# Kernel optimization log

Hardware: AMD Instinct MI355X
Metric: run time of the kernel (lower is better)

Reference implementation:

```python
import jax, jax.numpy as jnp
import numpy as np

B, T, C = 4, 2048, 2048
H = 16
D = C // H  # head_dim = 128


def setup_inputs() -> dict:
    key = jax.random.key(0)
    ks = jax.random.split(key, 11)
    s = 0.02
    return {
        "q": jax.random.normal(ks[0], (B, T, C), jnp.float32),
        "k": jax.random.normal(ks[1], (B, T, C), jnp.float32),
        "v": jax.random.normal(ks[2], (B, T, C), jnp.float32),
        "Wq": jax.random.normal(ks[3], (C, C), jnp.float32) * s,
        "bq": jnp.zeros((C,), jnp.float32),
        "Wk": jax.random.normal(ks[4], (C, C), jnp.float32) * s,
        "bk": jnp.zeros((C,), jnp.float32),
        "Wv": jax.random.normal(ks[5], (C, C), jnp.float32) * s,
        "bv": jnp.zeros((C,), jnp.float32),
        "Wo": jax.random.normal(ks[6], (C, C), jnp.float32) * s,
        "bo": jnp.zeros((C,), jnp.float32),
    }


def reference(q, k, v, Wq, bq, Wk, bk, Wv, bv, Wo, bo):
    # torch Linear: y = x @ W.T + b
    def heads(x, W, b):
        y = x @ W.T + b                      # [B,T,C]
        return y.reshape(B, T, H, D).transpose(0, 2, 1, 3)  # [B,H,T,D]

    q_h = heads(q, Wq, bq)
    k_h = heads(k, Wk, bk)
    v_h = heads(v, Wv, bv)

    scale = D ** -0.5
    scores = jnp.einsum('bhqd,bhkd->bhqk', q_h, k_h) * scale  # [B,H,T,T]
    # causal mask (is_causal=True)
    causal = jnp.tril(jnp.ones((T, T), dtype=bool))
    scores = jnp.where(causal, scores, -jnp.inf)
    probs = jax.nn.softmax(scores, axis=-1)
    out = jnp.einsum('bhqk,bhkd->bhqd', probs, v_h)           # [B,H,T,D]
    out = out.transpose(0, 2, 1, 3).reshape(B, T, C)
    return out @ Wo.T + bo
```

## Files before the change

### kernel.cpp

```cpp
#include <hip/hip_runtime.h>
#include <hip/hip_bf16.h>
#include <cmath>


#define DEV __device__ __forceinline__

typedef short short8 __attribute__((ext_vector_type(8)));
typedef float floatx4 __attribute__((ext_vector_type(4)));

#define LDS16(gp, lp)                                                        \
  __builtin_amdgcn_global_load_lds(                                          \
      (const __attribute__((address_space(1))) void*)(gp),                   \
      (__attribute__((address_space(3))) void*)(lp), 16, 0, 0)

DEV unsigned short f2bf(float f) {
  unsigned u = __builtin_bit_cast(unsigned, f);
  u += 0x7fffu + ((u >> 16) & 1u);
  return (unsigned short)(u >> 16);
}

DEV floatx4 mfma16(short8 a, short8 b, floatx4 c) {
  return __builtin_amdgcn_mfma_f32_16x16x32_bf16(a, b, c, 0, 0, 0);
}

struct Cvt7Args {
  const float* in[7];
  unsigned short* out[7];
  int n4[7];
};

__global__ __launch_bounds__(256) void cvt7_kernel(Cvt7Args a) {
  const int s = blockIdx.y;
  const float* __restrict__ in = a.in[s];
  unsigned short* __restrict__ out = a.out[s];
  const int n4 = a.n4[s];
  int stride = gridDim.x * blockDim.x;
  for (int i = blockIdx.x * blockDim.x + threadIdx.x; i < n4; i += stride) {
    float4 v = reinterpret_cast<const float4*>(in)[i];
    ushort4 o;
    o.x = f2bf(v.x); o.y = f2bf(v.y); o.z = f2bf(v.z); o.w = f2bf(v.w);
    reinterpret_cast<ushort4*>(out)[i] = o;
  }
}

DEV void gemm256_core(const unsigned short* __restrict__ aT,
                      const unsigned short* __restrict__ bT,
                      unsigned short* lds, const int K, floatx4 (&acc)[8][4]) {
  const int t = threadIdx.x;
  const int l = t & 63;
  const int w = t >> 6;
  const int wm = w >> 2, wn = w & 3;
  const int lr = l & 15, lg = l >> 4;
  const int NT = K >> 5;

  const int rA0 = t >> 2;
  const int chA0 = (t & 3) ^ ((rA0 >> 1) & 3);
  const int rA1 = (t + 512) >> 2;
  const int chA1 = (t & 3) ^ ((rA1 >> 1) & 3);

  auto stage = [&](int kt, int buf) {
    unsigned short* dst = lds + buf * 16384;
    const unsigned short* ga = aT + kt * 32;
    const unsigned short* gb = bT + kt * 32;
    LDS16(ga + (size_t)rA0 * K + chA0 * 8, dst + t * 8);
    LDS16(ga + (size_t)rA1 * K + chA1 * 8, dst + (t + 512) * 8);
    LDS16(gb + (size_t)rA0 * K + chA0 * 8, dst + 8192 + t * 8);
    LDS16(gb + (size_t)rA1 * K + chA1 * 8, dst + 8192 + (t + 512) * 8);
  };

  stage(0, 0);
  stage(1, 1);
  stage(2, 2);
  asm volatile("s_waitcnt vmcnt(8)" ::: "memory");
  __builtin_amdgcn_s_barrier();
  asm volatile("" ::: "memory");

  for (int tt = 0; tt < NT; ++tt) {
    const unsigned short* lA = lds + (tt & 3) * 16384;
    const unsigned short* lB = lA + 8192;
    if (tt + 3 < NT) stage(tt + 3, (tt + 3) & 3);
    short8 aF[8], bF[4];
#pragma unroll
    for (int ni = 0; ni < 4; ni++) {
      int row = wn * 64 + ni * 16 + lr;
      bF[ni] = *(const short8*)&lB[row * 32 + ((lg ^ ((row >> 1) & 3)) * 8)];
    }
#pragma unroll
    for (int mi = 0; mi < 8; mi++) {
      int row = wm * 128 + mi * 16 + lr;
      aF[mi] = *(const short8*)&lA[row * 32 + ((lg ^ ((row >> 1) & 3)) * 8)];
    }
    __builtin_amdgcn_s_setprio(1);
#pragma unroll
    for (int mi = 0; mi < 8; mi++)
#pragma unroll
      for (int ni = 0; ni < 4; ni++)
        acc[mi][ni] = mfma16(aF[mi], bF[ni], acc[mi][ni]);
    __builtin_amdgcn_s_setprio(0);
    if (tt + 1 < NT) {
      if (tt + 4 <= NT)
        asm volatile("s_waitcnt vmcnt(8)" ::: "memory");
      else if (tt + 3 == NT)
        asm volatile("s_waitcnt vmcnt(4)" ::: "memory");
      else
        asm volatile("s_waitcnt vmcnt(0)" ::: "memory");
      __builtin_amdgcn_s_barrier();
      asm volatile("" ::: "memory");
    }
  }
}

__global__ __launch_bounds__(512, 2) void gemm256_proj3(
    const unsigned short* __restrict__ qb, const unsigned short* __restrict__ kb,
    const unsigned short* __restrict__ vb, const unsigned short* __restrict__ wqb,
    const unsigned short* __restrict__ wkb, const unsigned short* __restrict__ wvb,
    const float* __restrict__ bq, const float* __restrict__ bk,
    const float* __restrict__ bv, unsigned short* __restrict__ Qp,
    unsigned short* __restrict__ Kp, unsigned short* __restrict__ Vt,
    float qscale) {
  constexpr int K = 2048, N = 2048;
  __shared__ unsigned short lds[65536];
  const int seg = blockIdx.x >> 8;
  int inner = blockIdx.x & 255;
  inner = (inner & 7) * 32 + (inner >> 3);
  const int bm = inner >> 3, bn = inner & 7;

  const unsigned short* A = (seg == 0) ? qb : (seg == 1) ? kb : vb;
  const unsigned short* Bw = (seg == 0) ? wqb : (seg == 1) ? wkb : wvb;
  const float* bias = (seg == 0) ? bq : (seg == 1) ? bk : bv;

  floatx4 zero = {0.f, 0.f, 0.f, 0.f};
  floatx4 acc[8][4];
#pragma unroll
  for (int i = 0; i < 8; i++)
#pragma unroll
    for (int j = 0; j < 4; j++) acc[i][j] = zero;

  gemm256_core(A + (size_t)bm * 256 * K, Bw + (size_t)bn * 256 * K, lds, K, acc);

  const int t = threadIdx.x, l = t & 63, w = t >> 6;
  const int wm = w >> 2, wn = w & 3;
  const int lr = l & 15, lg = l >> 4;
  const float oscale = (seg == 0) ? qscale : 1.0f;
  char* ldsb = (char*)lds;

  __syncthreads();

  if (seg < 2) {
#pragma unroll
    for (int ni = 0; ni < 4; ni++) {
      int col = wn * 64 + ni * 16 + lr;
      float bvv = bias[bn * 256 + col];
#pragma unroll
      for (int mi = 0; mi < 8; mi++) {
        int row0 = wm * 128 + mi * 16 + lg * 4;
#pragma unroll
        for (int r = 0; r < 4; r++) {
          int row = row0 + r;
          int off = row * 512 + ((col * 2) ^ (((row >> 2) & 15) << 5));
          *(unsigned short*)(ldsb + off) =
              f2bf((acc[mi][ni][r] + bvv) * oscale);
        }
      }
    }
    __syncthreads();
    unsigned short* dst = (seg == 0) ? Qp : Kp;
#pragma unroll
    for (int i = 0; i < 16; i++) {
      int c = i * 512 + t;
      int row = c >> 5, j = c & 31;
      int off = row * 512 + ((j * 16) ^ (((row >> 2) & 15) << 5));
      short8 v = *(const short8*)(ldsb + off);
      *(short8*)&dst[(size_t)(bm * 256 + row) * N + bn * 256 + j * 8] = v;
    }
  } else {
#pragma unroll
    for (int ni = 0; ni < 4; ni++) {
      int dp = wn * 64 + ni * 16 + lr;
      float bvv = bias[bn * 256 + dp];
#pragma unroll
      for (int mi = 0; mi < 8; mi++) {
        int tp0 = wm * 128 + mi * 16 + lg * 4;
        ushort4 v4;
        v4.x = f2bf(acc[mi][ni][0] + bvv);
        v4.y = f2bf(acc[mi][ni][1] + bvv);
        v4.z = f2bf(acc[mi][ni][2] + bvv);
        v4.w = f2bf(acc[mi][ni][3] + bvv);
        int off = dp * 512 + ((tp0 * 2) ^ ((dp & 15) << 5));
        *(ushort4*)(ldsb + off) = v4;
      }
    }
    __syncthreads();
    const int bb = bm >> 3;
    const int tb = (bm & 7) * 256;
#pragma unroll
    for (int i = 0; i < 16; i++) {
      int c = i * 512 + t;
      int dp = c >> 5, j = c & 31;
      int off = dp * 512 + ((j * 16) ^ ((dp & 15) << 5));
      short8 v = *(const short8*)(ldsb + off);
      int gcd = bn * 256 + dp;
      int h = gcd >> 7, d = gcd & 127;
      *(short8*)&Vt[((size_t)(bb * 16 + h) << 18) + (d << 11) + tb + j * 8] = v;
    }
  }
}

__global__ __launch_bounds__(512, 2) void gemm256_out(
    const unsigned short* __restrict__ A, const unsigned short* __restrict__ Bw,
    const float* __restrict__ bias, float* __restrict__ outp) {
  constexpr int K = 2048, N = 2048;
  __shared__ unsigned short lds[65536];
  int inner = blockIdx.x;
  inner = (inner & 7) * 32 + (inner >> 3);
  const int bm = inner >> 3, bn = inner & 7;

  floatx4 zero = {0.f, 0.f, 0.f, 0.f};
  floatx4 acc[8][4];
#pragma unroll
  for (int i = 0; i < 8; i++)
#pragma unroll
    for (int j = 0; j < 4; j++) acc[i][j] = zero;

  gemm256_core(A + (size_t)bm * 256 * K, Bw + (size_t)bn * 256 * K, lds, K, acc);

  const int t = threadIdx.x, l = t & 63, w = t >> 6;
  const int wm = w >> 2, wn = w & 3;
  const int lr = l & 15, lg = l >> 4;
  char* ldsb = (char*)lds;

  __syncthreads();

#pragma unroll
  for (int half = 0; half < 2; ++half) {
    if (wm == half) {
#pragma unroll
      for (int ni = 0; ni < 4; ni++) {
        int col = wn * 64 + ni * 16 + lr;
        float bvv = bias[bn * 256 + col];
#pragma unroll
        for (int mi = 0; mi < 8; mi++) {
          int lrow0 = mi * 16 + lg * 4;
#pragma unroll
          for (int r = 0; r < 4; r++) {
            int row = lrow0 + r;
            int off = row * 1024 + ((col * 4) ^ (((row >> 2) & 7) << 5));
            *(float*)(ldsb + off) = acc[mi][ni][r] + bvv;
          }
        }
      }
    }
    __syncthreads();
#pragma unroll
    for (int i = 0; i < 16; i++) {
      int c = i * 512 + t;
      int row = c >> 6, j = c & 63;
      int off = row * 1024 + ((j * 16) ^ (((row >> 2) & 7) << 5));
      float4 v = *(const float4*)(ldsb + off);
      *(float4*)&outp[(size_t)(bm * 256 + half * 128 + row) * N + bn * 256 +
                      j * 4] = v;
    }
    __syncthreads();
  }
}

__global__ __launch_bounds__(512, 2) void attn_kernel(
    const unsigned short* __restrict__ Qp, const unsigned short* __restrict__ Kp,
    const unsigned short* __restrict__ Vt, unsigned short* __restrict__ Out) {
  constexpr int T = 2048, C = 2048;
  __shared__ unsigned short lds[49152];
  unsigned short* sP = lds + 32768;

  const int bid = blockIdx.x;
  const int swz = (bid & 7) * 32 + (bid >> 3);
  const int bh = swz >> 2;
  const int pr = swz & 3;
  const int b = bh >> 4, h = bh & 15;
  const int t = threadIdx.x, l = t & 63, w = t >> 6;
  const int lr = l & 15, lg = l >> 4, l7 = l & 7;

  const unsigned short* Kg = Kp + (size_t)(b * T) * C + h * 128;
  const unsigned short* Vg = Vt + ((size_t)bh << 18);

  auto stage_kv = [&](int kb, int buf) {
    unsigned short* dK = lds + (buf ? 8192 : 0);
    unsigned short* dV = lds + 16384 + (buf ? 8192 : 0);
#pragma unroll
    for (int i = 0; i < 2; i++) {
      int c = t + i * 512;
      int row = c >> 4, cc = c & 15;
      LDS16(Kg + (size_t)(kb + row) * C + (cc ^ (row & 7)) * 8, &dK[c * 8]);
    }
#pragma unroll
    for (int i = 0; i < 2; i++) {
      int c = t + i * 512;
      int d = c >> 3, cc = c & 7;
      LDS16(Vg + (size_t)d * T + kb + (cc ^ (d & 7)) * 8, &dV[c * 8]);
    }
  };

  for (int seg = 0; seg < 2; seg++) {
    const int qs = seg ? pr : 7 - pr;
    const unsigned short* Qg = Qp + (size_t)(b * T + qs * 256) * C + h * 128;

#pragma unroll
    for (int i = 0; i < 8; i++) {
      int c = t + i * 512;
      int row = c >> 4, cc = c & 15;
      LDS16(Qg + (size_t)row * C + cc * 8, &lds[c * 8]);
    }
    __syncthreads();
    const int qw = qs * 256 + w * 32;
    short8 qf[2][4];
#pragma unroll
    for (int mi = 0; mi < 2; mi++)
#pragma unroll
      for (int ks = 0; ks < 4; ks++)
        qf[mi][ks] = *(const short8*)&lds[(w * 32 + mi * 16 + lr) * 128 +
                                          ks * 32 + lg * 8];
    __syncthreads();

    floatx4 zero = {0.f, 0.f, 0.f, 0.f};
    floatx4 oacc[2][8];
#pragma unroll
    for (int i = 0; i < 2; i++)
#pragma unroll
      for (int j = 0; j < 8; j++) oacc[i][j] = zero;
    float mold[2][4], lsum[2][4];
#pragma unroll
    for (int i = 0; i < 2; i++)
#pragma unroll
      for (int r = 0; r < 4; r++) { mold[i][r] = -1e30f; lsum[i][r] = 0.f; }

    const int ntile = 4 * qs + 4;
    stage_kv(0, 0);
    __syncthreads();
    int cur = 0;
    for (int tile = 0; tile < ntile; tile++) {
      const int kbase = tile * 64;
      if (tile + 1 < ntile) stage_kv(kbase + 64, cur ^ 1);
      const unsigned short* sK = lds + (cur ? 8192 : 0);
      const unsigned short* sV = lds + 16384 + (cur ? 8192 : 0);
      if (kbase <= qw + 31) {
        floatx4 sc[2][4];
#pragma unroll
        for (int i = 0; i < 2; i++)
#pragma unroll
          for (int j = 0; j < 4; j++) sc[i][j] = zero;
        __builtin_amdgcn_s_setprio(1);
#pragma unroll
        for (int ks = 0; ks < 4; ks++) {
#pragma unroll
          for (int ni = 0; ni < 4; ni++) {
            int R = ni * 16 + lr;
            short8 bF = *(const short8*)&sK[R * 128 + ((ks * 4 + lg) ^ l7) * 8];
#pragma unroll
            for (int mi = 0; mi < 2; mi++)
              sc[mi][ni] = mfma16(qf[mi][ks], bF, sc[mi][ni]);
          }
        }
        __builtin_amdgcn_s_setprio(0);
        if (kbase + 63 > qw) {
#pragma unroll
          for (int mi = 0; mi < 2; mi++)
#pragma unroll
            for (int ni = 0; ni < 4; ni++)
#pragma unroll
              for (int r = 0; r < 4; r++) {
                int col = kbase + ni * 16 + lr;
                int row = qw + mi * 16 + lg * 4 + r;
                if (col > row) sc[mi][ni][r] = -1e30f;
              }
        }
#pragma unroll
        for (int mi = 0; mi < 2; mi++) {
          float xr[4];
          int dok = 1;
#pragma unroll
          for (int r = 0; r < 4; r++) {
            float x = fmaxf(fmaxf(sc[mi][0][r], sc[mi][1][r]),
                            fmaxf(sc[mi][2][r], sc[mi][3][r]));
            x = fmaxf(x, __shfl_xor(x, 1));
            x = fmaxf(x, __shfl_xor(x, 2));
            x = fmaxf(x, __shfl_xor(x, 4));
            x = fmaxf(x, __shfl_xor(x, 8));
            xr[r] = x;
            dok &= (x - mold[mi][r] <= 8.0f) ? 1 : 0;
          }
          const bool defer = __all(dok);
          float al[4];
          if (!defer) {
#pragma unroll
            for (int r = 0; r < 4; r++) {
              float m2 = fmaxf(mold[mi][r], xr[r]);
              al[r] = __builtin_amdgcn_exp2f(mold[mi][r] - m2);
              mold[mi][r] = m2;
            }
          }
          float rs[4] = {0.f, 0.f, 0.f, 0.f};
#pragma unroll
          for (int ni = 0; ni < 4; ni++)
#pragma unroll
            for (int r = 0; r < 4; r++) {
              float p = __builtin_amdgcn_exp2f(sc[mi][ni][r] - mold[mi][r]);
              sc[mi][ni][r] = p;
              rs[r] += p;
            }
#pragma unroll
          for (int r = 0; r < 4; r++) {
            float s = rs[r];
            s += __shfl_xor(s, 1);
            s += __shfl_xor(s, 2);
            s += __shfl_xor(s, 4);
            s += __shfl_xor(s, 8);
            rs[r] = s;
          }
          if (!defer) {
#pragma unroll
            for (int r = 0; r < 4; r++)
              lsum[mi][r] = lsum[mi][r] * al[r] + rs[r];
#pragma unroll
            for (int ni = 0; ni < 8; ni++)
#pragma unroll
              for (int r = 0; r < 4; r++) oacc[mi][ni][r] *= al[r];
          } else {
#pragma unroll
            for (int r = 0; r < 4; r++) lsum[mi][r] += rs[r];
          }
#pragma unroll
          for (int ni = 0; ni < 4; ni++)
#pragma unroll
            for (int r = 0; r < 4; r++) {
              int rr = mi * 16 + lg * 4 + r;
              int ch = (ni * 2 + ((l >> 3) & 1)) ^ (rr & 7);
              sP[w * 2048 + rr * 64 + ch * 8 + l7] = f2bf(sc[mi][ni][r]);
            }
        }
        __builtin_amdgcn_s_setprio(1);
#pragma unroll
        for (int ks = 0; ks < 2; ks++) {
          short8 pf[2];
#pragma unroll
          for (int mi = 0; mi < 2; mi++)
            pf[mi] = *(const short8*)&sP[w * 2048 + (mi * 16 + lr) * 64 +
                                         ((ks * 4 + lg) ^ l7) * 8];
#pragma unroll
          for (int ni = 0; ni < 8; ni++) {
            int d = ni * 16 + lr;
            short8 vF = *(const short8*)&sV[d * 64 + ((ks * 4 + lg) ^ l7) * 8];
#pragma unroll
            for (int mi = 0; mi < 2; mi++)
              oacc[mi][ni] = mfma16(pf[mi], vF, oacc[mi][ni]);
          }
        }
        __builtin_amdgcn_s_setprio(0);
      }
      __syncthreads();
      cur ^= 1;
    }
    {
      char* ldsb = (char*)lds;
#pragma unroll
      for (int mi = 0; mi < 2; mi++) {
        float rl[4];
#pragma unroll
        for (int r = 0; r < 4; r++) rl[r] = 1.0f / lsum[mi][r];
#pragma unroll
        for (int ni = 0; ni < 8; ni++) {
          int col = ni * 16 + lr;
#pragma unroll
          for (int r = 0; r < 4; r++) {
            int row = w * 32 + mi * 16 + lg * 4 + r;
            int off = row * 256 + ((col * 2) ^ (((row >> 2) & 7) << 5));
            *(unsigned short*)(ldsb + off) = f2bf(oacc[mi][ni][r] * rl[r]);
          }
        }
      }
      __syncthreads();
      unsigned short* Og = Out + (size_t)(b * T + qs * 256) * C + h * 128;
#pragma unroll
      for (int i = 0; i < 8; i++) {
        int c = i * 512 + t;
        int row = c >> 4, j = c & 15;
        int off = row * 256 + ((j * 16) ^ (((row >> 2) & 7) << 5));
        short8 v = *(const short8*)(ldsb + off);
        *(short8*)&Og[(size_t)row * C + j * 8] = v;
      }
      __syncthreads();
    }
  }
}

extern "C" void kernel_launch(void* const* d_in, const int* in_sizes, int n_in,
                              void* d_out, int out_size, void* d_ws,
                              size_t ws_size, hipStream_t stream) {
  const float* q = (const float*)d_in[0];
  const float* k = (const float*)d_in[1];
  const float* v = (const float*)d_in[2];
  const float* Wq = (const float*)d_in[3];
  const float* bq = (const float*)d_in[4];
  const float* Wk = (const float*)d_in[5];
  const float* bk = (const float*)d_in[6];
  const float* Wv = (const float*)d_in[7];
  const float* bv = (const float*)d_in[8];
  const float* Wo = (const float*)d_in[9];
  const float* bo = (const float*)d_in[10];

  const int B = 4, T = 2048, C = 2048;
  const size_t E = (size_t)B * T * C;
  const size_t WE = (size_t)C * C;
  unsigned short* ws = (unsigned short*)d_ws;
  unsigned short* qb = ws;
  unsigned short* kb = ws + E;
  unsigned short* vb = ws + 2 * E;
  unsigned short* wqb = ws + 3 * E;
  unsigned short* wkb = wqb + WE;
  unsigned short* wvb = wqb + 2 * WE;
  unsigned short* wob = wqb + 3 * WE;
  unsigned short* Qp = ws + 4 * E;
  unsigned short* Kp = ws + 5 * E;
  unsigned short* Vtb = ws + 6 * E;
  unsigned short* attn = qb;

  Cvt7Args ca;
  ca.in[0] = q;  ca.out[0] = qb;  ca.n4[0] = (int)(E / 4);
  ca.in[1] = k;  ca.out[1] = kb;  ca.n4[1] = (int)(E / 4);
  ca.in[2] = v;  ca.out[2] = vb;  ca.n4[2] = (int)(E / 4);
  ca.in[3] = Wq; ca.out[3] = wqb; ca.n4[3] = (int)(WE / 4);
  ca.in[4] = Wk; ca.out[4] = wkb; ca.n4[4] = (int)(WE / 4);
  ca.in[5] = Wv; ca.out[5] = wvb; ca.n4[5] = (int)(WE / 4);
  ca.in[6] = Wo; ca.out[6] = wob; ca.n4[6] = (int)(WE / 4);
  cvt7_kernel<<<dim3(512, 7), 256, 0, stream>>>(ca);

  const float qscale = 1.4426950408889634f / sqrtf(128.0f);
  gemm256_proj3<<<768, 512, 0, stream>>>(qb, kb, vb, wqb, wkb, wvb, bq, bk, bv,
                                         Qp, Kp, Vtb, qscale);

  attn_kernel<<<256, 512, 0, stream>>>(Qp, Kp, Vtb, attn);

  gemm256_out<<<256, 512, 0, stream>>>(attn, wob, bo, (float*)d_out);
}
```

Before: 492.6 us.

## Split attention into one q-block per workgroup and shrink P staging for occupancy

The attention kernel no longer loops over two causal-balanced q-segments per workgroup. It launches 512 workgroups, each handling a single 256-row q block, with a remapped block index so that long and short segments interleave. The per-wave P staging buffer is halved by writing and consuming P in two 32-column phases, which cuts LDS to 80KB. Launch bounds are raised to 4 waves-per-EU to allow more resident blocks. The costs are more pressure on registers and the loss of the paired load balancing inside each block, which now depends on the hardware scheduler.

```diff
diff --git a/kernel.cpp b/kernel.cpp
--- a/kernel.cpp
+++ b/kernel.cpp
@@ -264,20 +264,23 @@
   }
 }
 
-__global__ __launch_bounds__(512, 2) void attn_kernel(
+__global__ __launch_bounds__(512, 4) void attn_kernel(
     const unsigned short* __restrict__ Qp, const unsigned short* __restrict__ Kp,
     const unsigned short* __restrict__ Vt, unsigned short* __restrict__ Out) {
   constexpr int T = 2048, C = 2048;
-  __shared__ unsigned short lds[49152];
-  unsigned short* sP = lds + 32768;
+  __shared__ unsigned short lds[40960];
 
   const int bid = blockIdx.x;
-  const int swz = (bid & 7) * 32 + (bid >> 3);
-  const int bh = swz >> 2;
-  const int pr = swz & 3;
+  const int u = (bid & 7) * 64 + (bid >> 3);
+  const int p = (u >> 6) * 32 + (u & 31);
+  const int g = (u >> 5) & 1;
+  const int bh = p >> 2;
+  const int pr = p & 3;
+  const int qs = g ? pr : 7 - pr;
   const int b = bh >> 4, h = bh & 15;
   const int t = threadIdx.x, l = t & 63, w = t >> 6;
   const int lr = l & 15, lg = l >> 4, l7 = l & 7;
+  unsigned short* sPw = lds + 32768 + w * 1024;
 
   const unsigned short* Kg = Kp + (size_t)(b * T) * C + h * 128;
   const unsigned short* Vg = Vt + ((size_t)bh << 18);
@@ -299,194 +302,196 @@
     }
   };
 
-  for (int seg = 0; seg < 2; seg++) {
-    const int qs = seg ? pr : 7 - pr;
-    const unsigned short* Qg = Qp + (size_t)(b * T + qs * 256) * C + h * 128;
-
+  const unsigned short* Qg = Qp + (size_t)(b * T + qs * 256) * C + h * 128;
+
+#pragma unroll
+  for (int i = 0; i < 8; i++) {
+    int c = t + i * 512;
+    int row = c >> 4, cc = c & 15;
+    LDS16(Qg + (size_t)row * C + cc * 8, &lds[c * 8]);
+  }
+  __syncthreads();
+  const int qw = qs * 256 + w * 32;
+  short8 qf[2][4];
+#pragma unroll
+  for (int mi = 0; mi < 2; mi++)
+#pragma unroll
+    for (int ks = 0; ks < 4; ks++)
+      qf[mi][ks] = *(const short8*)&lds[(w * 32 + mi * 16 + lr) * 128 +
+                                        ks * 32 + lg * 8];
+  __syncthreads();
+
+  floatx4 zero = {0.f, 0.f, 0.f, 0.f};
+  floatx4 oacc[2][8];
+#pragma unroll
+  for (int i = 0; i < 2; i++)
+#pragma unroll
+    for (int j = 0; j < 8; j++) oacc[i][j] = zero;
+  float mold[2][4], lsum[2][4];
+#pragma unroll
+  for (int i = 0; i < 2; i++)
+#pragma unroll
+    for (int r = 0; r < 4; r++) { mold[i][r] = -1e30f; lsum[i][r] = 0.f; }
+
+  const int ntile = 4 * qs + 4;
+  stage_kv(0, 0);
+  __syncthreads();
+  int cur = 0;
+  for (int tile = 0; tile < ntile; tile++) {
+    const int kbase = tile * 64;
+    if (tile + 1 < ntile) stage_kv(kbase + 64, cur ^ 1);
+    const unsigned short* sK = lds + (cur ? 8192 : 0);
+    const unsigned short* sV = lds + 16384 + (cur ? 8192 : 0);
+    if (kbase <= qw + 31) {
+      floatx4 sc[2][4];
+#pragma unroll
+      for (int i = 0; i < 2; i++)
+#pragma unroll
+        for (int j = 0; j < 4; j++) sc[i][j] = zero;
+      __builtin_amdgcn_s_setprio(1);
+#pragma unroll
+      for (int ks = 0; ks < 4; ks++) {
+#pragma unroll
+        for (int ni = 0; ni < 4; ni++) {
+          int R = ni * 16 + lr;
+          short8 bF = *(const short8*)&sK[R * 128 + ((ks * 4 + lg) ^ l7) * 8];
+#pragma unroll
+          for (int mi = 0; mi < 2; mi++)
+            sc[mi][ni] = mfma16(qf[mi][ks], bF, sc[mi][ni]);
+        }
+      }
+      __builtin_amdgcn_s_setprio(0);
+      if (kbase + 63 > qw) {
+#pragma unroll
+        for (int mi = 0; mi < 2; mi++)
+#pragma unroll
+          for (int ni = 0; ni < 4; ni++)
+#pragma unroll
+            for (int r = 0; r < 4; r++) {
+              int col = kbase + ni * 16 + lr;
+              int row = qw + mi * 16 + lg * 4 + r;
+              if (col > row) sc[mi][ni][r] = -1e30f;
+            }
+      }
+#pragma unroll
+      for (int mi = 0; mi < 2; mi++) {
+        float xr[4];
+        int dok = 1;
+#pragma unroll
+        for (int r = 0; r < 4; r++) {
+          float x = fmaxf(fmaxf(sc[mi][0][r], sc[mi][1][r]),
+                          fmaxf(sc[mi][2][r], sc[mi][3][r]));
+          x = fmaxf(x, __shfl_xor(x, 1));
+          x = fmaxf(x, __shfl_xor(x, 2));
+          x = fmaxf(x, __shfl_xor(x, 4));
+          x = fmaxf(x, __shfl_xor(x, 8));
+          xr[r] = x;
+          dok &= (x - mold[mi][r] <= 8.0f) ? 1 : 0;
+        }
+        const bool defer = __all(dok);
+        float al[4];
+        if (!defer) {
+#pragma unroll
+          for (int r = 0; r < 4; r++) {
+            float m2 = fmaxf(mold[mi][r], xr[r]);
+            al[r] = __builtin_amdgcn_exp2f(mold[mi][r] - m2);
+            mold[mi][r] = m2;
+          }
+        }
+        float rs[4] = {0.f, 0.f, 0.f, 0.f};
+#pragma unroll
+        for (int ni = 0; ni < 4; ni++)
+#pragma unroll
+          for (int r = 0; r < 4; r++) {
+            float p2 = __builtin_amdgcn_exp2f(sc[mi][ni][r] - mold[mi][r]);
+            sc[mi][ni][r] = p2;
+            rs[r] += p2;
+          }
+#pragma unroll
+        for (int r = 0; r < 4; r++) {
+          float s = rs[r];
+          s += __shfl_xor(s, 1);
+          s += __shfl_xor(s, 2);
+          s += __shfl_xor(s, 4);
+          s += __shfl_xor(s, 8);
+          rs[r] = s;
+        }
+        if (!defer) {
+#pragma unroll
+          for (int r = 0; r < 4; r++)
+            lsum[mi][r] = lsum[mi][r] * al[r] + rs[r];
+#pragma unroll
+          for (int ni = 0; ni < 8; ni++)
+#pragma unroll
+            for (int r = 0; r < 4; r++) oacc[mi][ni][r] *= al[r];
+        } else {
+#pragma unroll
+          for (int r = 0; r < 4; r++) lsum[mi][r] += rs[r];
+        }
+      }
+      __builtin_amdgcn_s_setprio(1);
+#pragma unroll
+      for (int ph = 0; ph < 2; ph++) {
+#pragma unroll
+        for (int mi = 0; mi < 2; mi++)
+#pragma unroll
+          for (int dn = 0; dn < 2; dn++)
+#pragma unroll
+            for (int r = 0; r < 4; r++) {
+              int ni = ph * 2 + dn;
+              int rr = mi * 16 + lg * 4 + r;
+              int lch = (dn * 2 + (lr >> 3)) ^ ((rr >> 1) & 3);
+              sPw[rr * 32 + lch * 8 + l7] = f2bf(sc[mi][ni][r]);
+            }
+        short8 pf[2];
+#pragma unroll
+        for (int mi = 0; mi < 2; mi++) {
+          int rr2 = mi * 16 + lr;
+          pf[mi] =
+              *(const short8*)&sPw[rr2 * 32 + ((lg ^ ((rr2 >> 1) & 3)) * 8)];
+        }
+#pragma unroll
+        for (int ni = 0; ni < 8; ni++) {
+          int d = ni * 16 + lr;
+          short8 vF =
+              *(const short8*)&sV[d * 64 + (((ph * 4 + lg) ^ l7) * 8)];
+#pragma unroll
+          for (int mi = 0; mi < 2; mi++)
+            oacc[mi][ni] = mfma16(pf[mi], vF, oacc[mi][ni]);
+        }
+      }
+      __builtin_amdgcn_s_setprio(0);
+    }
+    __syncthreads();
+    cur ^= 1;
+  }
+  {
+    char* ldsb = (char*)lds;
+#pragma unroll
+    for (int mi = 0; mi < 2; mi++) {
+      float rl[4];
+#pragma unroll
+      for (int r = 0; r < 4; r++) rl[r] = 1.0f / lsum[mi][r];
+#pragma unroll
+      for (int ni = 0; ni < 8; ni++) {
+        int col = ni * 16 + lr;
+#pragma unroll
+        for (int r = 0; r < 4; r++) {
+          int row = w * 32 + mi * 16 + lg * 4 + r;
+          int off = row * 256 + ((col * 2) ^ (((row >> 2) & 7) << 5));
+          *(unsigned short*)(ldsb + off) = f2bf(oacc[mi][ni][r] * rl[r]);
+        }
+      }
+    }
+    __syncthreads();
+    unsigned short* Og = Out + (size_t)(b * T + qs * 256) * C + h * 128;
 #pragma unroll
     for (int i = 0; i < 8; i++) {
-      int c = t + i * 512;
-      int row = c >> 4, cc = c & 15;
-      LDS16(Qg + (size_t)row * C + cc * 8, &lds[c * 8]);
-    }
-    __syncthreads();
-    const int qw = qs * 256 + w * 32;
-    short8 qf[2][4];
-#pragma unroll
-    for (int mi = 0; mi < 2; mi++)
-#pragma unroll
-      for (int ks = 0; ks < 4; ks++)
-        qf[mi][ks] = *(const short8*)&lds[(w * 32 + mi * 16 + lr) * 128 +
-                                          ks * 32 + lg * 8];
-    __syncthreads();
-
-    floatx4 zero = {0.f, 0.f, 0.f, 0.f};
-    floatx4 oacc[2][8];
-#pragma unroll
-    for (int i = 0; i < 2; i++)
-#pragma unroll
-      for (int j = 0; j < 8; j++) oacc[i][j] = zero;
-    float mold[2][4], lsum[2][4];
-#pragma unroll
-    for (int i = 0; i < 2; i++)
-#pragma unroll
-      for (int r = 0; r < 4; r++) { mold[i][r] = -1e30f; lsum[i][r] = 0.f; }
-
-    const int ntile = 4 * qs + 4;
-    stage_kv(0, 0);
-    __syncthreads();
-    int cur = 0;
-    for (int tile = 0; tile < ntile; tile++) {
-      const int kbase = tile * 64;
-      if (tile + 1 < ntile) stage_kv(kbase + 64, cur ^ 1);
-      const unsigned short* sK = lds + (cur ? 8192 : 0);
-      const unsigned short* sV = lds + 16384 + (cur ? 8192 : 0);
-      if (kbase <= qw + 31) {
-        floatx4 sc[2][4];
-#pragma unroll
-        for (int i = 0; i < 2; i++)
-#pragma unroll
-          for (int j = 0; j < 4; j++) sc[i][j] = zero;
-        __builtin_amdgcn_s_setprio(1);
-#pragma unroll
-        for (int ks = 0; ks < 4; ks++) {
-#pragma unroll
-          for (int ni = 0; ni < 4; ni++) {
-            int R = ni * 16 + lr;
-            short8 bF = *(const short8*)&sK[R * 128 + ((ks * 4 + lg) ^ l7) * 8];
-#pragma unroll
-            for (int mi = 0; mi < 2; mi++)
-              sc[mi][ni] = mfma16(qf[mi][ks], bF, sc[mi][ni]);
-          }
-        }
-        __builtin_amdgcn_s_setprio(0);
-        if (kbase + 63 > qw) {
-#pragma unroll
-          for (int mi = 0; mi < 2; mi++)
-#pragma unroll
-            for (int ni = 0; ni < 4; ni++)
-#pragma unroll
-              for (int r = 0; r < 4; r++) {
-                int col = kbase + ni * 16 + lr;
-                int row = qw + mi * 16 + lg * 4 + r;
-                if (col > row) sc[mi][ni][r] = -1e30f;
-              }
-        }
-#pragma unroll
-        for (int mi = 0; mi < 2; mi++) {
-          float xr[4];
-          int dok = 1;
-#pragma unroll
-          for (int r = 0; r < 4; r++) {
-            float x = fmaxf(fmaxf(sc[mi][0][r], sc[mi][1][r]),
-                            fmaxf(sc[mi][2][r], sc[mi][3][r]));
-            x = fmaxf(x, __shfl_xor(x, 1));
-            x = fmaxf(x, __shfl_xor(x, 2));
-            x = fmaxf(x, __shfl_xor(x, 4));
-            x = fmaxf(x, __shfl_xor(x, 8));
-            xr[r] = x;
-            dok &= (x - mold[mi][r] <= 8.0f) ? 1 : 0;
-          }
-          const bool defer = __all(dok);
-          float al[4];
-          if (!defer) {
-#pragma unroll
-            for (int r = 0; r < 4; r++) {
-              float m2 = fmaxf(mold[mi][r], xr[r]);
-              al[r] = __builtin_amdgcn_exp2f(mold[mi][r] - m2);
-              mold[mi][r] = m2;
-            }
-          }
-          float rs[4] = {0.f, 0.f, 0.f, 0.f};
-#pragma unroll
-          for (int ni = 0; ni < 4; ni++)
-#pragma unroll
-            for (int r = 0; r < 4; r++) {
-              float p = __builtin_amdgcn_exp2f(sc[mi][ni][r] - mold[mi][r]);
-              sc[mi][ni][r] = p;
-              rs[r] += p;
-            }
-#pragma unroll
-          for (int r = 0; r < 4; r++) {
-            float s = rs[r];
-            s += __shfl_xor(s, 1);
-            s += __shfl_xor(s, 2);
-            s += __shfl_xor(s, 4);
-            s += __shfl_xor(s, 8);
-            rs[r] = s;
-          }
-          if (!defer) {
-#pragma unroll
-            for (int r = 0; r < 4; r++)
-              lsum[mi][r] = lsum[mi][r] * al[r] + rs[r];
-#pragma unroll
-            for (int ni = 0; ni < 8; ni++)
-#pragma unroll
-              for (int r = 0; r < 4; r++) oacc[mi][ni][r] *= al[r];
-          } else {
-#pragma unroll
-            for (int r = 0; r < 4; r++) lsum[mi][r] += rs[r];
-          }
-#pragma unroll
-          for (int ni = 0; ni < 4; ni++)
-#pragma unroll
-            for (int r = 0; r < 4; r++) {
-              int rr = mi * 16 + lg * 4 + r;
-              int ch = (ni * 2 + ((l >> 3) & 1)) ^ (rr & 7);
-              sP[w * 2048 + rr * 64 + ch * 8 + l7] = f2bf(sc[mi][ni][r]);
-            }
-        }
-        __builtin_amdgcn_s_setprio(1);
-#pragma unroll
-        for (int ks = 0; ks < 2; ks++) {
-          short8 pf[2];
-#pragma unroll
-          for (int mi = 0; mi < 2; mi++)
-            pf[mi] = *(const short8*)&sP[w * 2048 + (mi * 16 + lr) * 64 +
-                                         ((ks * 4 + lg) ^ l7) * 8];
-#pragma unroll
-          for (int ni = 0; ni < 8; ni++) {
-            int d = ni * 16 + lr;
-            short8 vF = *(const short8*)&sV[d * 64 + ((ks * 4 + lg) ^ l7) * 8];
-#pragma unroll
-            for (int mi = 0; mi < 2; mi++)
-              oacc[mi][ni] = mfma16(pf[mi], vF, oacc[mi][ni]);
-          }
-        }
-        __builtin_amdgcn_s_setprio(0);
-      }
-      __syncthreads();
-      cur ^= 1;
-    }
-    {
-      char* ldsb = (char*)lds;
-#pragma unroll
-      for (int mi = 0; mi < 2; mi++) {
-        float rl[4];
-#pragma unroll
-        for (int r = 0; r < 4; r++) rl[r] = 1.0f / lsum[mi][r];
-#pragma unroll
-        for (int ni = 0; ni < 8; ni++) {
-          int col = ni * 16 + lr;
-#pragma unroll
-          for (int r = 0; r < 4; r++) {
-            int row = w * 32 + mi * 16 + lg * 4 + r;
-            int off = row * 256 + ((col * 2) ^ (((row >> 2) & 7) << 5));
-            *(unsigned short*)(ldsb + off) = f2bf(oacc[mi][ni][r] * rl[r]);
-          }
-        }
-      }
-      __syncthreads();
-      unsigned short* Og = Out + (size_t)(b * T + qs * 256) * C + h * 128;
-#pragma unroll
-      for (int i = 0; i < 8; i++) {
-        int c = i * 512 + t;
-        int row = c >> 4, j = c & 15;
-        int off = row * 256 + ((j * 16) ^ (((row >> 2) & 7) << 5));
-        short8 v = *(const short8*)(ldsb + off);
-        *(short8*)&Og[(size_t)row * C + j * 8] = v;
-      }
-      __syncthreads();
+      int c = i * 512 + t;
+      int row = c >> 4, j = c & 15;
+      int off = row * 256 + ((j * 16) ^ (((row >> 2) & 7) << 5));
+      short8 v = *(const short8*)(ldsb + off);
+      *(short8*)&Og[(size_t)row * C + j * 8] = v;
     }
   }
 }
@@ -536,7 +541,7 @@
   gemm256_proj3<<<768, 512, 0, stream>>>(qb, kb, vb, wqb, wkb, wvb, bq, bk, bv,
                                          Qp, Kp, Vtb, qscale);
 
-  attn_kernel<<<256, 512, 0, stream>>>(Qp, Kp, Vtb, attn);
+  attn_kernel<<<512, 512, 0, stream>>>(Qp, Kp, Vtb, attn);
 
   gemm256_out<<<256, 512, 0, stream>>>(attn, wob, bo, (float*)d_out);
 }
```

After: 761.7 us. 1.55x slower.
